# Optimization experiments

Hardware: AMD Instinct MI355X
Metric: run time of the kernel (lower is better)

The kernel has to match this reference:

```python
import jax, jax.numpy as jnp
import numpy as np

N, C, H, W = 32, 512, 64, 64
R = 16
CB = C // R  # bottleneck channels = 32
EPS = 1e-5


def setup_inputs() -> dict:
    key = jax.random.key(0)
    ks = jax.random.split(key, 5)
    return {
        "x": jax.random.normal(ks[0], (N, C, H, W), dtype=jnp.float32),
        "wk_w": jax.random.normal(ks[1], (C,), dtype=jnp.float32) * (1.0 / np.sqrt(C)),
        "wk_b": jax.random.normal(ks[2], (1,), dtype=jnp.float32) * 0.01,
        "wv1_w": jax.random.normal(ks[3], (CB, C), dtype=jnp.float32) * (1.0 / np.sqrt(C)),
        "ln_g": jnp.ones((CB,), dtype=jnp.float32),
        "ln_b": jnp.zeros((CB,), dtype=jnp.float32),
        "wv2_w": jax.random.normal(ks[4], (C, CB), dtype=jnp.float32) * (1.0 / np.sqrt(CB)),
    }


def reference(x, wk_w, wk_b, wv1_w, ln_g, ln_b, wv2_w):
    # x: (n, c, h, w)
    # attention logits via 1x1 conv (c -> 1): (n, h, w)
    logits = jnp.einsum("nchw,c->nhw", x, wk_w) + wk_b[0]
    # Faithful to original: F.softmax(dim=2) on (n,1,h,w) -> softmax over H only
    attn = jax.nn.softmax(logits, axis=1)  # (n, h, w)
    # context pooling: (n, c, hw) @ (n, hw, 1) -> (n, c)
    ctx = jnp.einsum("nchw,nhw->nc", x, attn)
    # bottleneck: conv1x1 (c -> c/r), LayerNorm over channel, ReLU, conv1x1 (c/r -> c)
    v = ctx @ wv1_w.T  # (n, c/r)
    mu = jnp.mean(v, axis=-1, keepdims=True)
    var = jnp.mean((v - mu) ** 2, axis=-1, keepdims=True)
    v = (v - mu) * jax.lax.rsqrt(var + EPS) * ln_g + ln_b
    v = jax.nn.relu(v)
    out = v @ wv2_w.T  # (n, c)
    return out[:, :, None, None] + x
```

## Files before the change

### kernel.cpp

```cpp
#include <hip/hip_runtime.h>

#define N 32
#define C 512
#define H 64
#define W 64
#define HW 4096
#define CB 32
#define NCHUNK 4
#define CCHUNK 128
#define EPS 1e-5f

__global__ __launch_bounds__(256) void k1_logits_partial(
    const float* __restrict__ x, const float* __restrict__ wk_w,
    float* __restrict__ partial)
{
    const int tid   = threadIdx.x;
    const int tile  = blockIdx.x;
    const int chunk = blockIdx.y;
    const int n     = blockIdx.z;
    const int hw4   = tile * 256 + tid;
    const float4* xb = (const float4*)(x + (size_t)n * C * HW);
    const int c0 = chunk * CCHUNK;
    float4 acc = make_float4(0.f, 0.f, 0.f, 0.f);
    #pragma unroll 4
    for (int c = 0; c < CCHUNK; ++c) {
        const float wv = wk_w[c0 + c];
        const float4 xv = xb[(size_t)(c0 + c) * (HW / 4) + hw4];
        acc.x += xv.x * wv; acc.y += xv.y * wv;
        acc.z += xv.z * wv; acc.w += xv.w * wv;
    }
    float4* pb = (float4*)(partial + (size_t)(n * NCHUNK + chunk) * HW);
    pb[hw4] = acc;
}

__global__ __launch_bounds__(256) void k2_softmax(
    const float* __restrict__ partial, const float* __restrict__ wk_b,
    float* __restrict__ attn)
{
    const int tid  = threadIdx.x;
    const int lane = tid & 63;
    const int wid  = blockIdx.x * 4 + (tid >> 6);
    const int n = wid >> 6;
    const int w = wid & 63;
    float l = wk_b[0];
    #pragma unroll
    for (int ch = 0; ch < NCHUNK; ++ch)
        l += partial[(size_t)(n * NCHUNK + ch) * HW + lane * W + w];
    float m = l;
    #pragma unroll
    for (int o = 32; o > 0; o >>= 1) m = fmaxf(m, __shfl_xor(m, o));
    const float e = __expf(l - m);
    float s = e;
    #pragma unroll
    for (int o = 32; o > 0; o >>= 1) s += __shfl_xor(s, o);
    attn[(size_t)n * HW + lane * W + w] = e / s;
}

__global__ __launch_bounds__(256) void k3_ctx(
    const float* __restrict__ x, const float* __restrict__ attn,
    float* __restrict__ ctx)
{
    const int tid  = threadIdx.x;
    const int lane = tid & 63;
    const int wid  = blockIdx.x * 4 + (tid >> 6);
    const int n = wid >> 9;
    const float4* xr = (const float4*)(x + (size_t)wid * HW);
    const float4* ar = (const float4*)(attn + (size_t)n * HW);
    float acc = 0.f;
    #pragma unroll
    for (int i = 0; i < 16; ++i) {
        const float4 xv = xr[i * 64 + lane];
        const float4 av = ar[i * 64 + lane];
        acc += xv.x * av.x + xv.y * av.y + xv.z * av.z + xv.w * av.w;
    }
    #pragma unroll
    for (int o = 32; o > 0; o >>= 1) acc += __shfl_xor(acc, o);
    if (lane == 0) ctx[wid] = acc;
}

__global__ __launch_bounds__(256) void k4_bottleneck(
    const float* __restrict__ ctx, const float* __restrict__ wv1_w,
    const float* __restrict__ ln_g, const float* __restrict__ ln_b,
    const float* __restrict__ wv2_w, float* __restrict__ out_vec)
{
    __shared__ float ctx_s[C];
    __shared__ float v_s[CB];
    const int tid = threadIdx.x;
    const int n   = blockIdx.x;
    ctx_s[tid]       = ctx[n * C + tid];
    ctx_s[tid + 256] = ctx[n * C + tid + 256];
    __syncthreads();
    {
        const int b = tid >> 3, sub = tid & 7;
        const float* wr = wv1_w + b * C;
        float s = 0.f;
        #pragma unroll 8
        for (int j = sub; j < C; j += 8) s += wr[j] * ctx_s[j];
        #pragma unroll
        for (int o = 4; o > 0; o >>= 1) s += __shfl_down(s, o, 8);
        if (sub == 0) v_s[b] = s;
    }
    __syncthreads();
    if (tid < CB) {
        const float val = v_s[tid];
        float sm = val, sq = val * val;
        #pragma unroll
        for (int o = 16; o > 0; o >>= 1) {
            sm += __shfl_xor(sm, o, 32);
            sq += __shfl_xor(sq, o, 32);
        }
        const float mu  = sm / CB;
        const float var = sq / CB - mu * mu;
        const float vh  = (val - mu) * rsqrtf(var + EPS) * ln_g[tid] + ln_b[tid];
        v_s[tid] = fmaxf(vh, 0.f);
    }
    __syncthreads();
    for (int c = tid; c < C; c += 256) {
        const float* w2 = wv2_w + c * CB;
        float a = 0.f;
        #pragma unroll
        for (int b = 0; b < CB; ++b) a += v_s[b] * w2[b];
        out_vec[n * C + c] = a;
    }
}

__global__ __launch_bounds__(256) void k5_add(
    const float* __restrict__ x, const float* __restrict__ out_vec,
    float* __restrict__ out)
{
    const size_t i4 = (size_t)blockIdx.x * 256 + threadIdx.x;
    const int nc = (int)(i4 >> 10);
    const float4 xv = ((const float4*)x)[i4];
    const float a = out_vec[nc];
    ((float4*)out)[i4] = make_float4(xv.x + a, xv.y + a, xv.z + a, xv.w + a);
}

extern "C" void kernel_launch(void* const* d_in, const int* in_sizes, int n_in,
                              void* d_out, int out_size, void* d_ws, size_t ws_size,
                              hipStream_t stream) {
    const float* x     = (const float*)d_in[0];
    const float* wk_w  = (const float*)d_in[1];
    const float* wk_b  = (const float*)d_in[2];
    const float* wv1_w = (const float*)d_in[3];
    const float* ln_g  = (const float*)d_in[4];
    const float* ln_b  = (const float*)d_in[5];
    const float* wv2_w = (const float*)d_in[6];
    float* out = (float*)d_out;

    float* ws      = (float*)d_ws;
    float* partial = ws;
    float* attn    = partial + (size_t)N * NCHUNK * HW;
    float* ctx     = attn + (size_t)N * HW;
    float* ovec    = ctx + (size_t)N * C;

    k1_logits_partial<<<dim3(4, 4, 32), 256, 0, stream>>>(x, wk_w, partial);
    k2_softmax<<<512, 256, 0, stream>>>(partial, wk_b, attn);
    k3_ctx<<<4096, 256, 0, stream>>>(x, attn, ctx);
    k4_bottleneck<<<32, 256, 0, stream>>>(ctx, wv1_w, ln_g, ln_b, wv2_w, ovec);
    k5_add<<<65536, 256, 0, stream>>>(x, ovec, out);
}
```

Baseline: 535.6 us.

## Split logits over more channel chunks, batch ctx rows, nontemporal add kernel

The logits partial kernel now uses 8 channel chunks of 64 instead of 4 of 128, doubling its grid to expose more parallelism. The context kernel has each wave compute four channels, reusing each attention load across four rows of x and storing the results as one float4. The final add kernel gives each block one (n,c) plane with four float4 iterations and uses nontemporal loads and stores to avoid cache pollution. Together these aim to cut launch and load overhead on bandwidth-bound passes, at the cost of more partial-sum traffic in the softmax step and fewer, heavier blocks.

```diff
diff --git a/kernel.cpp b/kernel.cpp
--- a/kernel.cpp
+++ b/kernel.cpp
@@ -6,26 +6,27 @@
 #define W 64
 #define HW 4096
 #define CB 32
-#define NCHUNK 4
-#define CCHUNK 128
+#define NCHUNK 8
+#define CCHUNK 64
 #define EPS 1e-5f
+
+typedef float fvec4 __attribute__((ext_vector_type(4)));
 
 __global__ __launch_bounds__(256) void k1_logits_partial(
     const float* __restrict__ x, const float* __restrict__ wk_w,
     float* __restrict__ partial)
 {
     const int tid   = threadIdx.x;
-    const int tile  = blockIdx.x;
+    const int hw4   = blockIdx.x * 256 + tid;
     const int chunk = blockIdx.y;
     const int n     = blockIdx.z;
-    const int hw4   = tile * 256 + tid;
-    const float4* xb = (const float4*)(x + (size_t)n * C * HW);
-    const int c0 = chunk * CCHUNK;
+    const int c0    = chunk * CCHUNK;
+    const float4* xb = (const float4*)(x + ((size_t)n * C + c0) * HW);
     float4 acc = make_float4(0.f, 0.f, 0.f, 0.f);
-    #pragma unroll 4
+    #pragma unroll 8
     for (int c = 0; c < CCHUNK; ++c) {
         const float wv = wk_w[c0 + c];
-        const float4 xv = xb[(size_t)(c0 + c) * (HW / 4) + hw4];
+        const float4 xv = xb[(size_t)c * (HW / 4) + hw4];
         acc.x += xv.x * wv; acc.y += xv.y * wv;
         acc.z += xv.z * wv; acc.w += xv.w * wv;
     }
@@ -62,20 +63,35 @@
 {
     const int tid  = threadIdx.x;
     const int lane = tid & 63;
-    const int wid  = blockIdx.x * 4 + (tid >> 6);
-    const int n = wid >> 9;
-    const float4* xr = (const float4*)(x + (size_t)wid * HW);
+    const int g    = blockIdx.x * 4 + (tid >> 6);
+    const int n    = g >> 7;
+    const int c0   = (g & 127) * 4;
     const float4* ar = (const float4*)(attn + (size_t)n * HW);
-    float acc = 0.f;
+    const float4* xr = (const float4*)(x + ((size_t)n * C + c0) * HW);
+    float a0 = 0.f, a1 = 0.f, a2 = 0.f, a3 = 0.f;
     #pragma unroll
     for (int i = 0; i < 16; ++i) {
-        const float4 xv = xr[i * 64 + lane];
-        const float4 av = ar[i * 64 + lane];
-        acc += xv.x * av.x + xv.y * av.y + xv.z * av.z + xv.w * av.w;
+        const int idx = i * 64 + lane;
+        const float4 av = ar[idx];
+        const float4 x0 = xr[idx];
+        const float4 x1 = xr[1024 + idx];
+        const float4 x2 = xr[2048 + idx];
+        const float4 x3 = xr[3072 + idx];
+        a0 += x0.x * av.x + x0.y * av.y + x0.z * av.z + x0.w * av.w;
+        a1 += x1.x * av.x + x1.y * av.y + x1.z * av.z + x1.w * av.w;
+        a2 += x2.x * av.x + x2.y * av.y + x2.z * av.z + x2.w * av.w;
+        a3 += x3.x * av.x + x3.y * av.y + x3.z * av.z + x3.w * av.w;
     }
     #pragma unroll
-    for (int o = 32; o > 0; o >>= 1) acc += __shfl_xor(acc, o);
-    if (lane == 0) ctx[wid] = acc;
+    for (int o = 32; o > 0; o >>= 1) {
+        a0 += __shfl_xor(a0, o);
+        a1 += __shfl_xor(a1, o);
+        a2 += __shfl_xor(a2, o);
+        a3 += __shfl_xor(a3, o);
+    }
+    if (lane == 0) {
+        *(float4*)(ctx + (size_t)n * C + c0) = make_float4(a0, a1, a2, a3);
+    }
 }
 
 __global__ __launch_bounds__(256) void k4_bottleneck(
@@ -128,11 +144,18 @@
     const float* __restrict__ x, const float* __restrict__ out_vec,
     float* __restrict__ out)
 {
-    const size_t i4 = (size_t)blockIdx.x * 256 + threadIdx.x;
-    const int nc = (int)(i4 >> 10);
-    const float4 xv = ((const float4*)x)[i4];
+    const int tid = threadIdx.x;
+    const int nc  = blockIdx.x;
+    const fvec4* xp = (const fvec4*)x + (size_t)nc * (HW / 4);
+    fvec4*       op = (fvec4*)out     + (size_t)nc * (HW / 4);
     const float a = out_vec[nc];
-    ((float4*)out)[i4] = make_float4(xv.x + a, xv.y + a, xv.z + a, xv.w + a);
+    #pragma unroll
+    for (int i = 0; i < 4; ++i) {
+        const int idx = i * 256 + tid;
+        fvec4 v = __builtin_nontemporal_load(xp + idx);
+        v += a;
+        __builtin_nontemporal_store(v, op + idx);
+    }
 }
 
 extern "C" void kernel_launch(void* const* d_in, const int* in_sizes, int n_in,
@@ -153,9 +176,9 @@
     float* ctx     = attn + (size_t)N * HW;
     float* ovec    = ctx + (size_t)N * C;
 
-    k1_logits_partial<<<dim3(4, 4, 32), 256, 0, stream>>>(x, wk_w, partial);
+    k1_logits_partial<<<dim3(4, NCHUNK, 32), 256, 0, stream>>>(x, wk_w, partial);
     k2_softmax<<<512, 256, 0, stream>>>(partial, wk_b, attn);
-    k3_ctx<<<4096, 256, 0, stream>>>(x, attn, ctx);
+    k3_ctx<<<1024, 256, 0, stream>>>(x, attn, ctx);
     k4_bottleneck<<<32, 256, 0, stream>>>(ctx, wv1_w, ln_g, ln_b, wv2_w, ovec);
-    k5_add<<<65536, 256, 0, stream>>>(x, ovec, out);
+    k5_add<<<16384, 256, 0, stream>>>(x, ovec, out);
 }
```

After: 543.1 us. About the same (+1.4%).
